# Kernel tuning notes

Measured on AMD Instinct MI355X. Metric: run time of the kernel, lower is better.

The kernel has to match this reference:

```python
import jax, jax.numpy as jnp
import numpy as np

B, N, D, H, F = 16, 512, 768, 12, 3072
HD = D // H
EPS = 1e-5
NEG_INF = -1e30  # stand-in for -inf; softmax of all -inf rows handled via nan_to_num semantics


def layer_norm(x, g, b):
    mu = jnp.mean(x, axis=-1, keepdims=True)
    var = jnp.mean(jnp.square(x - mu), axis=-1, keepdims=True)
    return (x - mu) * jax.lax.rsqrt(var + EPS) * g + b


def setup_inputs() -> dict:
    key = jax.random.key(0)
    ks = jax.random.split(key, 16)
    s = 0.02
    return {
        "x": jax.random.normal(ks[0], (B, N, D), jnp.float32),
        "spatial_encoding": jax.random.normal(ks[1], (B, N, N), jnp.float32),
        "edge_encoding": jax.random.normal(ks[2], (B, N, N), jnp.float32),
        "Wq": jax.random.normal(ks[3], (D, D), jnp.float32) * s,
        "Wk": jax.random.normal(ks[4], (D, D), jnp.float32) * s,
        "Wv": jax.random.normal(ks[5], (D, D), jnp.float32) * s,
        "bv": jnp.zeros((D,), jnp.float32),
        "Wo": jax.random.normal(ks[6], (D, D), jnp.float32) * s,
        "bo": jnp.zeros((D,), jnp.float32),
        "g1": jnp.ones((D,), jnp.float32),
        "be1": jnp.zeros((D,), jnp.float32),
        "g2": jnp.ones((D,), jnp.float32),
        "be2": jnp.zeros((D,), jnp.float32),
        "W1": jax.random.normal(ks[7], (D, F), jnp.float32) * s,
        "bf1": jnp.zeros((F,), jnp.float32),
        "W2": jax.random.normal(ks[8], (F, D), jnp.float32) * s,
        "bf2": jnp.zeros((D,), jnp.float32),
    }


def reference(x, spatial_encoding, edge_encoding, Wq, Wk, Wv, bv, Wo, bo,
              g1, be1, g2, be2, W1, bf1, W2, bf2):
    scale = D ** (-0.5)
    h = layer_norm(x, g1, be1)                              # n1(x)
    bias = (spatial_encoding + edge_encoding)[:, None]      # [B,1,N,N]

    q = (h @ Wq).reshape(B, N, H, HD).transpose(0, 2, 1, 3)  # [B,H,N,hd]
    k = (h @ Wk).reshape(B, N, H, HD).transpose(0, 2, 1, 3)
    v = (h @ Wv + bv).reshape(B, N, H, HD).transpose(0, 2, 1, 3)

    a = jnp.einsum('bhqd,bhkd->bhqk', q, k) * scale + bias   # [B,H,N,N]
    # pad rows (all-zero score rows) get -inf -> softmax NaN -> nan_to_num -> 0
    row_nonzero = jnp.any(a != 0, axis=-1, keepdims=True)
    a = jnp.where(row_nonzero, a, NEG_INF)
    p = jax.nn.softmax(a, axis=-1)
    p = jnp.where(row_nonzero, p, 0.0)  # mirrors nan_to_num on all -inf rows

    o = jnp.einsum('bhqk,bhkd->bhqd', p, v)                  # [B,H,N,hd]
    o = o.transpose(0, 2, 1, 3).reshape(B, N, D)
    att_output = o @ Wo + bo + x                              # residual

    pad_mask = jnp.any(att_output == 0, axis=-1)              # [B,N]
    ffn_in = layer_norm(x, g2, be2)                           # note: n2(x), as in source
    hmid = jax.nn.gelu(ffn_in @ W1 + bf1, approximate=True)
    ffn_out = hmid @ W2 + bf2 + att_output
    return jnp.where(pad_mask[..., None], 0.0, ffn_out)
```

## Files before the change

### kernel.cpp

```cpp
#include <hip/hip_runtime.h>
#include <math.h>

typedef unsigned short u16;
typedef __bf16 bf16x8 __attribute__((ext_vector_type(8)));
typedef float f32x4 __attribute__((ext_vector_type(4)));

__device__ __forceinline__ u16 f2bf(float f){
  union{float f; unsigned u;} v; v.f = f;
  return (u16)((v.u + 0x7fffu + ((v.u >> 16) & 1u)) >> 16);
}
__device__ __forceinline__ float bf2f(u16 b){
  union{unsigned u; float f;} v; v.u = (unsigned)b << 16; return v.f;
}

#define LOG2E 1.4426950408889634f

__global__ void prep_weights(const float* __restrict__ Wq, const float* __restrict__ Wk,
                             const float* __restrict__ Wv, const float* __restrict__ Wo,
                             const float* __restrict__ W1, const float* __restrict__ W2,
                             const float* __restrict__ g1, const float* __restrict__ g2,
                             u16* __restrict__ WqkvT, u16* __restrict__ WoT,
                             u16* __restrict__ W1T, u16* __restrict__ W2T, float qscale){
  __shared__ float t[32][33];
  int bid = blockIdx.x;
  const float* src; u16* dst; const float* rs; float sc; int R, C, bx, by;
  if (bid < 576)      {            src=Wq; dst=WqkvT;          rs=g1;      sc=qscale; R=768;  C=768;  bx=bid%24; by=bid/24; }
  else if (bid <1152) { bid-=576;  src=Wk; dst=WqkvT+768*768;  rs=g1;      sc=1.f;    R=768;  C=768;  bx=bid%24; by=bid/24; }
  else if (bid <1728) { bid-=1152; src=Wv; dst=WqkvT+1536*768; rs=g1;      sc=1.f;    R=768;  C=768;  bx=bid%24; by=bid/24; }
  else if (bid <2304) { bid-=1728; src=Wo; dst=WoT;            rs=nullptr; sc=1.f;    R=768;  C=768;  bx=bid%24; by=bid/24; }
  else if (bid <4608) { bid-=2304; src=W1; dst=W1T;            rs=g2;      sc=1.f;    R=768;  C=3072; bx=bid%96; by=bid/96; }
  else                { bid-=4608; src=W2; dst=W2T;            rs=nullptr; sc=1.f;    R=3072; C=768;  bx=bid%24; by=bid/24; }
  int c0 = bx * 32, r0 = by * 32;
  int tx = threadIdx.x, ty = threadIdx.y;
  #pragma unroll
  for (int i = 0; i < 4; i++)
    t[ty + i*8][tx] = src[(size_t)(r0 + ty + i*8) * C + c0 + tx];
  __syncthreads();
  float fac = (rs ? rs[r0 + tx] : 1.f) * sc;
  #pragma unroll
  for (int i = 0; i < 4; i++)
    dst[(size_t)(c0 + ty + i*8) * R + r0 + tx] = f2bf(t[tx][ty + i*8] * fac);
}

__global__ __launch_bounds__(256) void fold_bias(
    const float* __restrict__ Wq, const float* __restrict__ Wk,
    const float* __restrict__ Wv, const float* __restrict__ W1,
    const float* __restrict__ be1, const float* __restrict__ be2,
    const float* __restrict__ bv, const float* __restrict__ bf1,
    float* __restrict__ qkvb, float* __restrict__ bf1f){
  __shared__ float red[4][64];
  int tx = threadIdx.x & 63, ty = threadIdx.x >> 6;
  int j = blockIdx.x * 64 + tx;
  const float* W; int col, stride; const float* bvec;
  if (j < 768)       { W = Wq; col = j;        stride = 768;  bvec = be1; }
  else if (j < 1536) { W = Wk; col = j - 768;  stride = 768;  bvec = be1; }
  else if (j < 2304) { W = Wv; col = j - 1536; stride = 768;  bvec = be1; }
  else               { W = W1; col = j - 2304; stride = 3072; bvec = be2; }
  float s = 0.f;
  for (int k = ty * 192; k < (ty + 1) * 192; k++)
    s += bvec[k] * W[(size_t)k * stride + col];
  red[ty][tx] = s;
  __syncthreads();
  if (ty == 0){
    s = red[0][tx] + red[1][tx] + red[2][tx] + red[3][tx];
    if (j < 1536)      qkvb[j] = s;
    else if (j < 2304) qkvb[j] = s + bv[col];
    else               bf1f[col] = s + bf1[col];
  }
}

__global__ void bias_prep(u16* __restrict__ dst, const float* __restrict__ sp,
                          const float* __restrict__ ed){
  int t = blockIdx.x * blockDim.x + threadIdx.x;
  int row = t >> 7, c0 = (t & 127) * 4;
  size_t base = (size_t)row * 512;
  float4 s = *(const float4*)&sp[base + c0];
  float4 e = *(const float4*)&ed[base + c0];
  int kt = c0 >> 7, cw = c0 & 127, fk = cw >> 4, l0 = cw & 15;
  u16* o = dst + base + kt*128 + fk;
  o[(l0+0)*8] = f2bf((s.x+e.x)*LOG2E);
  o[(l0+1)*8] = f2bf((s.y+e.y)*LOG2E);
  o[(l0+2)*8] = f2bf((s.z+e.z)*LOG2E);
  o[(l0+3)*8] = f2bf((s.w+e.w)*LOG2E);
}

__global__ __launch_bounds__(256) void ln_kernel(
    const float* __restrict__ x, u16* __restrict__ hn){
  const int lane = threadIdx.x & 63, wave = threadIdx.x >> 6;
  const int row = blockIdx.x * 4 + wave;
  const float4* xr = (const float4*)(x + (size_t)row * 768);
  float4 v[3];
  float sum = 0.f, sq = 0.f;
  #pragma unroll
  for (int c = 0; c < 3; c++){
    v[c] = xr[lane + 64*c];
    sum += v[c].x + v[c].y + v[c].z + v[c].w;
    sq  += v[c].x*v[c].x + v[c].y*v[c].y + v[c].z*v[c].z + v[c].w*v[c].w;
  }
  #pragma unroll
  for (int d = 1; d < 64; d <<= 1){ sum += __shfl_xor(sum, d); sq += __shfl_xor(sq, d); }
  float mu  = sum * (1.f/768.f);
  float var = sq * (1.f/768.f) - mu*mu;
  float rs  = rsqrtf(var + 1e-5f);
  #pragma unroll
  for (int c = 0; c < 3; c++){
    int f4 = lane + 64*c;
    ushort4 o{f2bf((v[c].x-mu)*rs), f2bf((v[c].y-mu)*rs),
              f2bf((v[c].z-mu)*rs), f2bf((v[c].w-mu)*rs)};
    ((ushort4*)(hn + (size_t)row*768))[f4] = o;
  }
}

template<int EPI>
__global__ __launch_bounds__(256, 2) void gemm_bt(
    const u16* __restrict__ A, const u16* __restrict__ Bt, void* __restrict__ Cout,
    const float* __restrict__ bias, const void* __restrict__ resid,
    u16* __restrict__ vt, int M, int Nn, int K){
  __shared__ __align__(16) u16 As[128*64];
  __shared__ __align__(16) u16 Bs[128*64];
  const int tid = threadIdx.x, lane = tid & 63, wave = tid >> 6;
  const int wm = wave >> 1, wn = wave & 1;
  const int l15 = lane & 15, lg = lane >> 4;
  const int bid = blockIdx.y * gridDim.x + blockIdx.x;
  const int cpx = (gridDim.x * gridDim.y) >> 3;
  const int swz = (bid & 7) * cpx + (bid >> 3);
  const int m0 = (swz / gridDim.x) * 128, n0 = (swz % gridDim.x) * 128;
  f32x4 acc[4][4] = {};
  for (int k0 = 0; k0 < K; k0 += 64){
    #pragma unroll
    for (int i = 0; i < 4; i++){
      int chunk = i*256 + tid;
      int row = chunk >> 3, seg = (chunk & 7) ^ (row & 7);
      __builtin_amdgcn_global_load_lds(
        (const __attribute__((address_space(1))) void*)&A[(size_t)(m0+row)*K + k0 + seg*8],
        (__attribute__((address_space(3))) void*)&As[(size_t)(i*256 + wave*64)*8], 16, 0, 0);
      __builtin_amdgcn_global_load_lds(
        (const __attribute__((address_space(1))) void*)&Bt[(size_t)(n0+row)*K + k0 + seg*8],
        (__attribute__((address_space(3))) void*)&Bs[(size_t)(i*256 + wave*64)*8], 16, 0, 0);
    }
    __syncthreads();
    bf16x8 af[4][2], bfr[4][2];
    #pragma unroll
    for (int i = 0; i < 4; i++){
      int ra = wm*64 + i*16 + l15, rb = wn*64 + i*16 + l15;
      #pragma unroll
      for (int kk = 0; kk < 2; kk++){
        af[i][kk]  = *(const bf16x8*)&As[ra*64 + (((kk*4 + lg) ^ (l15 & 7)) << 3)];
        bfr[i][kk] = *(const bf16x8*)&Bs[rb*64 + (((kk*4 + lg) ^ (l15 & 7)) << 3)];
      }
    }
    #pragma unroll
    for (int kk = 0; kk < 2; kk++)
      #pragma unroll
      for (int i = 0; i < 4; i++)
        #pragma unroll
        for (int j = 0; j < 4; j++)
          acc[i][j] = __builtin_amdgcn_mfma_f32_16x16x32_bf16(af[i][kk], bfr[j][kk], acc[i][j], 0, 0, 0);
    __syncthreads();
  }
  #pragma unroll
  for (int i = 0; i < 4; i++){
    int row_base = m0 + wm*64 + i*16 + lg*4;
    #pragma unroll
    for (int j = 0; j < 4; j++){
      int col = n0 + wn*64 + j*16 + l15;
      float bcol = bias ? bias[col] : 0.f;
      if (EPI == 5 && col >= 1536){
        int hv = (col - 1536) >> 6, hd = (col - 1536) & 63;
        int b = row_base >> 9, n = row_base & 511;
        int within = n & 127;
        int newn = (n & ~127) + ((((within >> 3) ^ (hd & 7)) << 3)) + (within & 7);
        ushort4 ov{f2bf(acc[i][j][0] + bcol), f2bf(acc[i][j][1] + bcol),
                   f2bf(acc[i][j][2] + bcol), f2bf(acc[i][j][3] + bcol)};
        *(ushort4*)&vt[(((size_t)(b*12 + hv)*64 + hd) << 9) + newn] = ov;
        continue;
      }
      #pragma unroll
      for (int r = 0; r < 4; r++){
        size_t idx = (size_t)(row_base + r) * Nn + col;
        float v = acc[i][j][r] + bcol;
        if (EPI == 3){
          v += ((const float*)resid)[idx];
          ((u16*)Cout)[idx] = f2bf(v);
        } else if (EPI == 4){
          v += bf2f(((const u16*)resid)[idx]);
          ((float*)Cout)[idx] = v;
        } else if (EPI == 2){
          float u = v + 0.044715f * v * v * v;
          float e = exp2f(-2.3022182f * u);
          ((u16*)Cout)[idx] = f2bf(v * __builtin_amdgcn_rcpf(1.f + e));
        } else {
          ((u16*)Cout)[idx] = f2bf(v);
        }
      }
    }
  }
}

__device__ __forceinline__ void attn_body(
    int bid, u16* sm, const u16* __restrict__ qkv, const u16* __restrict__ VTg,
    const u16* __restrict__ biasPb, u16* __restrict__ Og){
  u16* Ks = sm;
  u16* Vs = sm + 8192;
  u16* Pl = sm + 16384;
  const int tid = threadIdx.x, lane = tid & 63, wave = tid >> 6;
  const int l15 = lane & 15, lg = lane >> 4;
  const int swz = (bid & 7) * 96 + (bid >> 3);
  const int bh = swz >> 2, b = bh / 12, h = bh % 12;
  const int q0 = (swz & 3) * 128 + wave * 32;
  const u16* Qb = qkv + (size_t)b * 512 * 2304 + h * 64;
  const u16* Kb = Qb + 768;
  const u16* Vbh = VTg + (size_t)bh * 64 * 512;
  u16* Pw = &Pl[wave * 32 * 136];

  bf16x8 qf[2][2];
  #pragma unroll
  for (int fm = 0; fm < 2; fm++)
    #pragma unroll
    for (int kk = 0; kk < 2; kk++)
      qf[fm][kk] = *(const bf16x8*)&Qb[(size_t)(q0 + fm*16 + l15)*2304 + kk*32 + lg*8];

  f32x4 O[2][4] = {};
  float lrow[2][4] = {};

  for (int kt = 0; kt < 4; kt++){
    const int k0 = kt * 128;
    bf16x8 bb[2][4];
    #pragma unroll
    for (int fm = 0; fm < 2; fm++)
      #pragma unroll
      for (int r = 0; r < 4; r++){
        int qrow = q0 + fm*16 + lg*4 + r;
        bb[fm][r] = *(const bf16x8*)&biasPb[((size_t)(b*512 + qrow)*4 + kt)*128 + l15*8];
      }
    #pragma unroll
    for (int i = 0; i < 4; i++){
      int chunk = i*256 + tid;
      int r = chunk >> 3, cc = chunk & 7;
      __builtin_amdgcn_global_load_lds(
        (const __attribute__((address_space(1))) void*)&Kb[(size_t)(k0 + r)*2304 + ((cc ^ (r & 7)) << 3)],
        (__attribute__((address_space(3))) void*)&Ks[(size_t)(i*256 + wave*64)*8],
        16, 0, 0);
    }
    #pragma unroll
    for (int i = 0; i < 4; i++){
      int chunk = i*256 + tid;
      int r = chunk >> 4, cc = chunk & 15;
      __builtin_amdgcn_global_load_lds(
        (const __attribute__((address_space(1))) void*)&Vbh[(size_t)r*512 + k0 + (cc << 3)],
        (__attribute__((address_space(3))) void*)&Vs[(size_t)(i*256 + wave*64)*8],
        16, 0, 0);
    }
    __syncthreads();

    f32x4 S[2][8] = {};
    #pragma unroll
    for (int fk = 0; fk < 8; fk++)
      #pragma unroll
      for (int kk = 0; kk < 2; kk++){
        int row = fk*16 + l15;
        bf16x8 kf = *(const bf16x8*)&Ks[row*64 + (((kk*4 + lg) ^ (l15 & 7)) << 3)];
        S[0][fk] = __builtin_amdgcn_mfma_f32_16x16x32_bf16(qf[0][kk], kf, S[0][fk], 0,0,0);
        S[1][fk] = __builtin_amdgcn_mfma_f32_16x16x32_bf16(qf[1][kk], kf, S[1][fk], 0,0,0);
      }
    #pragma unroll
    for (int fm = 0; fm < 2; fm++)
      #pragma unroll
      for (int r = 0; r < 4; r++){
        float rs = 0.f;
        #pragma unroll
        for (int fk = 0; fk < 8; fk++){
          float p = exp2f(S[fm][fk][r] + (float)bb[fm][r][fk]);
          S[fm][fk][r] = p;
          rs += p;
        }
        rs += __shfl_xor(rs, 1); rs += __shfl_xor(rs, 2);
        rs += __shfl_xor(rs, 4); rs += __shfl_xor(rs, 8);
        lrow[fm][r] += rs;
      }
    #pragma unroll
    for (int fm = 0; fm < 2; fm++)
      #pragma unroll
      for (int fk = 0; fk < 8; fk++)
        #pragma unroll
        for (int r = 0; r < 4; r++)
          Pw[(fm*16 + lg*4 + r)*136 + fk*16 + l15] = f2bf(S[fm][fk][r]);
    bf16x8 pf[2][4];
    #pragma unroll
    for (int fm = 0; fm < 2; fm++)
      #pragma unroll
      for (int kk = 0; kk < 4; kk++)
        pf[fm][kk] = *(const bf16x8*)&Pw[(fm*16 + l15)*136 + kk*32 + lg*8];
    #pragma unroll
    for (int fn = 0; fn < 4; fn++)
      #pragma unroll
      for (int kk = 0; kk < 4; kk++){
        int row = fn*16 + l15;
        bf16x8 vf = *(const bf16x8*)&Vs[row*128 + (((kk*4 + lg) ^ (l15 & 7)) << 3)];
        O[0][fn] = __builtin_amdgcn_mfma_f32_16x16x32_bf16(pf[0][kk], vf, O[0][fn], 0,0,0);
        O[1][fn] = __builtin_amdgcn_mfma_f32_16x16x32_bf16(pf[1][kk], vf, O[1][fn], 0,0,0);
      }
    __syncthreads();
  }
  #pragma unroll
  for (int fm = 0; fm < 2; fm++)
    #pragma unroll
    for (int r = 0; r < 4; r++){
      float inv = __builtin_amdgcn_rcpf(lrow[fm][r]);
      int qrow = q0 + fm*16 + lg*4 + r;
      #pragma unroll
      for (int fn = 0; fn < 4; fn++)
        Og[((size_t)b*512 + qrow)*768 + h*64 + fn*16 + l15] = f2bf(O[fm][fn][r] * inv);
    }
}

__device__ __forceinline__ void ffn1_body(
    int fid, u16* sm, const u16* __restrict__ A, const u16* __restrict__ Bt,
    u16* __restrict__ Cout, const float* __restrict__ bias){
  u16* As = sm;
  u16* Bs = sm + 8192;
  const int Nn = 3072, K = 768;
  const int tid = threadIdx.x, lane = tid & 63, wave = tid >> 6;
  const int wm = wave >> 1, wn = wave & 1;
  const int l15 = lane & 15, lg = lane >> 4;
  const int swz = (fid & 7) * 192 + (fid >> 3);
  const int m0 = (swz / 24) * 128, n0 = (swz % 24) * 128;
  f32x4 acc[4][4] = {};
  for (int k0 = 0; k0 < K; k0 += 64){
    #pragma unroll
    for (int i = 0; i < 4; i++){
      int chunk = i*256 + tid;
      int row = chunk >> 3, seg = (chunk & 7) ^ (row & 7);
      __builtin_amdgcn_global_load_lds(
        (const __attribute__((address_space(1))) void*)&A[(size_t)(m0+row)*K + k0 + seg*8],
        (__attribute__((address_space(3))) void*)&As[(size_t)(i*256 + wave*64)*8], 16, 0, 0);
      __builtin_amdgcn_global_load_lds(
        (const __attribute__((address_space(1))) void*)&Bt[(size_t)(n0+row)*K + k0 + seg*8],
        (__attribute__((address_space(3))) void*)&Bs[(size_t)(i*256 + wave*64)*8], 16, 0, 0);
    }
    __syncthreads();
    bf16x8 af[4][2], bfr[4][2];
    #pragma unroll
    for (int i = 0; i < 4; i++){
      int ra = wm*64 + i*16 + l15, rb = wn*64 + i*16 + l15;
      #pragma unroll
      for (int kk = 0; kk < 2; kk++){
        af[i][kk]  = *(const bf16x8*)&As[ra*64 + (((kk*4 + lg) ^ (l15 & 7)) << 3)];
        bfr[i][kk] = *(const bf16x8*)&Bs[rb*64 + (((kk*4 + lg) ^ (l15 & 7)) << 3)];
      }
    }
    #pragma unroll
    for (int kk = 0; kk < 2; kk++)
      #pragma unroll
      for (int i = 0; i < 4; i++)
        #pragma unroll
        for (int j = 0; j < 4; j++)
          acc[i][j] = __builtin_amdgcn_mfma_f32_16x16x32_bf16(af[i][kk], bfr[j][kk], acc[i][j], 0, 0, 0);
    __syncthreads();
  }
  #pragma unroll
  for (int i = 0; i < 4; i++){
    int row_base = m0 + wm*64 + i*16 + lg*4;
    #pragma unroll
    for (int j = 0; j < 4; j++){
      int col = n0 + wn*64 + j*16 + l15;
      float bcol = bias[col];
      #pragma unroll
      for (int r = 0; r < 4; r++){
        size_t idx = (size_t)(row_base + r) * Nn + col;
        float v = acc[i][j][r] + bcol;
        float u = v + 0.044715f * v * v * v;
        float e = exp2f(-2.3022182f * u);
        Cout[idx] = f2bf(v * __builtin_amdgcn_rcpf(1.f + e));
      }
    }
  }
}

__global__ __launch_bounds__(256, 2) void attn_ffn1(
    const u16* __restrict__ qkv, const u16* __restrict__ VTg,
    const u16* __restrict__ biasPb, u16* __restrict__ Og,
    const u16* __restrict__ hn, const u16* __restrict__ W1T,
    u16* __restrict__ Gg, const float* __restrict__ bf1f){
  __shared__ __align__(16) u16 sm[33792];
  const int bid = blockIdx.x;
  const int t = bid / 3, r = bid - t * 3;
  if (r == 0) attn_body(t, sm, qkv, VTg, biasPb, Og);
  else        ffn1_body(2*t + (r-1), sm, hn, W1T, Gg, bf1f);
}

extern "C" void kernel_launch(void* const* d_in, const int* in_sizes, int n_in,
                              void* d_out, int out_size, void* d_ws, size_t ws_size,
                              hipStream_t stream){
  const float* x   = (const float*)d_in[0];
  const float* sp  = (const float*)d_in[1];
  const float* ed  = (const float*)d_in[2];
  const float* Wq  = (const float*)d_in[3];
  const float* Wk  = (const float*)d_in[4];
  const float* Wv  = (const float*)d_in[5];
  const float* bv  = (const float*)d_in[6];
  const float* Wo  = (const float*)d_in[7];
  const float* bo  = (const float*)d_in[8];
  const float* g1  = (const float*)d_in[9];
  const float* be1 = (const float*)d_in[10];
  const float* g2  = (const float*)d_in[11];
  const float* be2 = (const float*)d_in[12];
  const float* W1  = (const float*)d_in[13];
  const float* bf1 = (const float*)d_in[14];
  const float* W2  = (const float*)d_in[15];
  const float* bf2 = (const float*)d_in[16];

  char* w = (char*)d_ws;
  size_t off = 0;
  auto alloc = [&](size_t bytes)->void*{ void* p = w + off; off += (bytes + 255) & ~(size_t)255; return p; };
  u16*   Gg    = (u16*)  alloc(8192ull*3072*2);
  u16*   qkv   = (u16*)  alloc(8192ull*2304*2);
  u16*   attb  = qkv;
  u16*   VTg   = (u16*)  alloc(8192ull*768*2);
  u16*   hn    = (u16*)  alloc(8192ull*768*2);
  u16*   Og    = (u16*)  alloc(8192ull*768*2);
  u16*   biasPb= (u16*)  alloc(16ull*512*512*2);
  u16*   WqkvT = (u16*)  alloc(2304ull*768*2);
  u16*   WoT   = (u16*)  alloc(768ull*768*2);
  u16*   W1T   = (u16*)  alloc(3072ull*768*2);
  u16*   W2T   = (u16*)  alloc(768ull*3072*2);
  float* qkvb  = (float*)alloc(2304ull*4);
  float* bf1f  = (float*)alloc(3072ull*4);

  const float qscale = 0.03608439182435161f * LOG2E;

  prep_weights<<<6912, dim3(32,8), 0, stream>>>(Wq, Wk, Wv, Wo, W1, W2, g1, g2,
                                                WqkvT, WoT, W1T, W2T, qscale);
  fold_bias<<<84, 256, 0, stream>>>(Wq, Wk, Wv, W1, be1, be2, bv, bf1, qkvb, bf1f);
  bias_prep<<<4096, 256, 0, stream>>>(biasPb, sp, ed);

  ln_kernel<<<2048, 256, 0, stream>>>(x, hn);

  gemm_bt<5><<<dim3(18,64),256,0,stream>>>(hn, WqkvT, qkv, qkvb, nullptr, VTg, 8192, 2304, 768);

  attn_ffn1<<<2304, 256, 0, stream>>>(qkv, VTg, biasPb, Og, hn, W1T, Gg, bf1f);

  gemm_bt<3><<<dim3(6,64),256,0,stream>>>(Og, WoT, attb, bo, x, nullptr, 8192, 768, 768);

  gemm_bt<4><<<dim3(6,64),256,0,stream>>>(Gg, W2T, (float*)d_out, bf2, attb, nullptr, 8192, 768, 3072);
}
```

Before: 255.3 us.

## Merge prep kernels and fuse Wo and W2 GEMMs into one concatenated-K GEMM

Combines bias prep, weight transpose, bias folding and LayerNorm into a single launch with block-range dispatch. The output projection and the second FFN GEMM become one GEMM that loops over a concatenated K range (Gg·W2T then Og·WoT). The epilogue adds the folded bias bo+bf2 and the residual x directly. This removes the bf16 attb intermediate round-trip and two kernel launches. The trade-off is a longer serial K loop per tile and a dispatch-heavy prep kernel.

```diff
diff --git a/kernel.cpp b/kernel.cpp
--- a/kernel.cpp
+++ b/kernel.cpp
@@ -9,113 +9,117 @@
   union{float f; unsigned u;} v; v.f = f;
   return (u16)((v.u + 0x7fffu + ((v.u >> 16) & 1u)) >> 16);
 }
-__device__ __forceinline__ float bf2f(u16 b){
-  union{unsigned u; float f;} v; v.u = (unsigned)b << 16; return v.f;
-}
 
 #define LOG2E 1.4426950408889634f
 
-__global__ void prep_weights(const float* __restrict__ Wq, const float* __restrict__ Wk,
-                             const float* __restrict__ Wv, const float* __restrict__ Wo,
-                             const float* __restrict__ W1, const float* __restrict__ W2,
-                             const float* __restrict__ g1, const float* __restrict__ g2,
-                             u16* __restrict__ WqkvT, u16* __restrict__ WoT,
-                             u16* __restrict__ W1T, u16* __restrict__ W2T, float qscale){
-  __shared__ float t[32][33];
-  int bid = blockIdx.x;
-  const float* src; u16* dst; const float* rs; float sc; int R, C, bx, by;
-  if (bid < 576)      {            src=Wq; dst=WqkvT;          rs=g1;      sc=qscale; R=768;  C=768;  bx=bid%24; by=bid/24; }
-  else if (bid <1152) { bid-=576;  src=Wk; dst=WqkvT+768*768;  rs=g1;      sc=1.f;    R=768;  C=768;  bx=bid%24; by=bid/24; }
-  else if (bid <1728) { bid-=1152; src=Wv; dst=WqkvT+1536*768; rs=g1;      sc=1.f;    R=768;  C=768;  bx=bid%24; by=bid/24; }
-  else if (bid <2304) { bid-=1728; src=Wo; dst=WoT;            rs=nullptr; sc=1.f;    R=768;  C=768;  bx=bid%24; by=bid/24; }
-  else if (bid <4608) { bid-=2304; src=W1; dst=W1T;            rs=g2;      sc=1.f;    R=768;  C=3072; bx=bid%96; by=bid/96; }
-  else                { bid-=4608; src=W2; dst=W2T;            rs=nullptr; sc=1.f;    R=3072; C=768;  bx=bid%24; by=bid/24; }
-  int c0 = bx * 32, r0 = by * 32;
-  int tx = threadIdx.x, ty = threadIdx.y;
-  #pragma unroll
-  for (int i = 0; i < 4; i++)
-    t[ty + i*8][tx] = src[(size_t)(r0 + ty + i*8) * C + c0 + tx];
-  __syncthreads();
-  float fac = (rs ? rs[r0 + tx] : 1.f) * sc;
-  #pragma unroll
-  for (int i = 0; i < 4; i++)
-    dst[(size_t)(c0 + ty + i*8) * R + r0 + tx] = f2bf(t[tx][ty + i*8] * fac);
-}
-
-__global__ __launch_bounds__(256) void fold_bias(
+__global__ __launch_bounds__(256) void prep_all(
+    const float* __restrict__ sp, const float* __restrict__ ed,
     const float* __restrict__ Wq, const float* __restrict__ Wk,
-    const float* __restrict__ Wv, const float* __restrict__ W1,
+    const float* __restrict__ Wv, const float* __restrict__ Wo,
+    const float* __restrict__ W1, const float* __restrict__ W2,
+    const float* __restrict__ g1, const float* __restrict__ g2,
     const float* __restrict__ be1, const float* __restrict__ be2,
     const float* __restrict__ bv, const float* __restrict__ bf1,
-    float* __restrict__ qkvb, float* __restrict__ bf1f){
+    const float* __restrict__ bo, const float* __restrict__ bf2,
+    const float* __restrict__ x,
+    u16* __restrict__ biasPb, u16* __restrict__ WqkvT, u16* __restrict__ WoT,
+    u16* __restrict__ W1T, u16* __restrict__ W2T,
+    float* __restrict__ qkvb, float* __restrict__ bf1f, float* __restrict__ bo2,
+    u16* __restrict__ hn, float qscale){
+  __shared__ float t[32][33];
   __shared__ float red[4][64];
-  int tx = threadIdx.x & 63, ty = threadIdx.x >> 6;
-  int j = blockIdx.x * 64 + tx;
-  const float* W; int col, stride; const float* bvec;
-  if (j < 768)       { W = Wq; col = j;        stride = 768;  bvec = be1; }
-  else if (j < 1536) { W = Wk; col = j - 768;  stride = 768;  bvec = be1; }
-  else if (j < 2304) { W = Wv; col = j - 1536; stride = 768;  bvec = be1; }
-  else               { W = W1; col = j - 2304; stride = 3072; bvec = be2; }
-  float s = 0.f;
-  for (int k = ty * 192; k < (ty + 1) * 192; k++)
-    s += bvec[k] * W[(size_t)k * stride + col];
-  red[ty][tx] = s;
-  __syncthreads();
-  if (ty == 0){
-    s = red[0][tx] + red[1][tx] + red[2][tx] + red[3][tx];
-    if (j < 1536)      qkvb[j] = s;
-    else if (j < 2304) qkvb[j] = s + bv[col];
-    else               bf1f[col] = s + bf1[col];
-  }
-}
-
-__global__ void bias_prep(u16* __restrict__ dst, const float* __restrict__ sp,
-                          const float* __restrict__ ed){
-  int t = blockIdx.x * blockDim.x + threadIdx.x;
-  int row = t >> 7, c0 = (t & 127) * 4;
-  size_t base = (size_t)row * 512;
-  float4 s = *(const float4*)&sp[base + c0];
-  float4 e = *(const float4*)&ed[base + c0];
-  int kt = c0 >> 7, cw = c0 & 127, fk = cw >> 4, l0 = cw & 15;
-  u16* o = dst + base + kt*128 + fk;
-  o[(l0+0)*8] = f2bf((s.x+e.x)*LOG2E);
-  o[(l0+1)*8] = f2bf((s.y+e.y)*LOG2E);
-  o[(l0+2)*8] = f2bf((s.z+e.z)*LOG2E);
-  o[(l0+3)*8] = f2bf((s.w+e.w)*LOG2E);
-}
-
-__global__ __launch_bounds__(256) void ln_kernel(
-    const float* __restrict__ x, u16* __restrict__ hn){
-  const int lane = threadIdx.x & 63, wave = threadIdx.x >> 6;
-  const int row = blockIdx.x * 4 + wave;
-  const float4* xr = (const float4*)(x + (size_t)row * 768);
-  float4 v[3];
-  float sum = 0.f, sq = 0.f;
-  #pragma unroll
-  for (int c = 0; c < 3; c++){
-    v[c] = xr[lane + 64*c];
-    sum += v[c].x + v[c].y + v[c].z + v[c].w;
-    sq  += v[c].x*v[c].x + v[c].y*v[c].y + v[c].z*v[c].z + v[c].w*v[c].w;
-  }
-  #pragma unroll
-  for (int d = 1; d < 64; d <<= 1){ sum += __shfl_xor(sum, d); sq += __shfl_xor(sq, d); }
-  float mu  = sum * (1.f/768.f);
-  float var = sq * (1.f/768.f) - mu*mu;
-  float rs  = rsqrtf(var + 1e-5f);
-  #pragma unroll
-  for (int c = 0; c < 3; c++){
-    int f4 = lane + 64*c;
-    ushort4 o{f2bf((v[c].x-mu)*rs), f2bf((v[c].y-mu)*rs),
-              f2bf((v[c].z-mu)*rs), f2bf((v[c].w-mu)*rs)};
-    ((ushort4*)(hn + (size_t)row*768))[f4] = o;
-  }
-}
-
-template<int EPI>
-__global__ __launch_bounds__(256, 2) void gemm_bt(
-    const u16* __restrict__ A, const u16* __restrict__ Bt, void* __restrict__ Cout,
-    const float* __restrict__ bias, const void* __restrict__ resid,
-    u16* __restrict__ vt, int M, int Nn, int K){
+  const int gbid = blockIdx.x, tid = threadIdx.x;
+
+  if (gbid < 4096){
+    int tt = gbid * 256 + tid;
+    int row = tt >> 7, c0 = (tt & 127) * 4;
+    size_t base = (size_t)row * 512;
+    float4 s = *(const float4*)&sp[base + c0];
+    float4 e = *(const float4*)&ed[base + c0];
+    int kt = c0 >> 7, cw = c0 & 127, fk = cw >> 4, l0 = cw & 15;
+    u16* o = biasPb + base + kt*128 + fk;
+    o[(l0+0)*8] = f2bf((s.x+e.x)*LOG2E);
+    o[(l0+1)*8] = f2bf((s.y+e.y)*LOG2E);
+    o[(l0+2)*8] = f2bf((s.z+e.z)*LOG2E);
+    o[(l0+3)*8] = f2bf((s.w+e.w)*LOG2E);
+  } else if (gbid < 11008){
+    int bid = gbid - 4096;
+    const float* src; u16* dst; const float* rs; float sc; int R, C, bx, by;
+    if (bid < 576)      {            src=Wq; dst=WqkvT;          rs=g1;      sc=qscale; R=768;  C=768;  bx=bid%24; by=bid/24; }
+    else if (bid <1152) { bid-=576;  src=Wk; dst=WqkvT+768*768;  rs=g1;      sc=1.f;    R=768;  C=768;  bx=bid%24; by=bid/24; }
+    else if (bid <1728) { bid-=1152; src=Wv; dst=WqkvT+1536*768; rs=g1;      sc=1.f;    R=768;  C=768;  bx=bid%24; by=bid/24; }
+    else if (bid <2304) { bid-=1728; src=Wo; dst=WoT;            rs=nullptr; sc=1.f;    R=768;  C=768;  bx=bid%24; by=bid/24; }
+    else if (bid <4608) { bid-=2304; src=W1; dst=W1T;            rs=g2;      sc=1.f;    R=768;  C=3072; bx=bid%96; by=bid/96; }
+    else                { bid-=4608; src=W2; dst=W2T;            rs=nullptr; sc=1.f;    R=3072; C=768;  bx=bid%24; by=bid/24; }
+    int c0 = bx * 32, r0 = by * 32;
+    int tx = tid & 31, ty = tid >> 5;
+    #pragma unroll
+    for (int i = 0; i < 4; i++)
+      t[ty + i*8][tx] = src[(size_t)(r0 + ty + i*8) * C + c0 + tx];
+    __syncthreads();
+    float fac = (rs ? rs[r0 + tx] : 1.f) * sc;
+    #pragma unroll
+    for (int i = 0; i < 4; i++)
+      dst[(size_t)(c0 + ty + i*8) * R + r0 + tx] = f2bf(t[tx][ty + i*8] * fac);
+  } else if (gbid < 11104){
+    int fbid = gbid - 11008;
+    int tx = tid & 63, ty = tid >> 6;
+    int j = fbid * 64 + tx;
+    if (j < 5376){
+      const float* W; int col, stride; const float* bvec;
+      if (j < 768)       { W = Wq; col = j;        stride = 768;  bvec = be1; }
+      else if (j < 1536) { W = Wk; col = j - 768;  stride = 768;  bvec = be1; }
+      else if (j < 2304) { W = Wv; col = j - 1536; stride = 768;  bvec = be1; }
+      else               { W = W1; col = j - 2304; stride = 3072; bvec = be2; }
+      float s = 0.f;
+      for (int k = ty * 192; k < (ty + 1) * 192; k++)
+        s += bvec[k] * W[(size_t)k * stride + col];
+      red[ty][tx] = s;
+    }
+    __syncthreads();
+    if (ty == 0){
+      if (j < 5376){
+        float s = red[0][tx] + red[1][tx] + red[2][tx] + red[3][tx];
+        if (j < 1536)      qkvb[j] = s;
+        else if (j < 2304) qkvb[j] = s + bv[j - 1536];
+        else               bf1f[j - 2304] = s + bf1[j - 2304];
+      } else {
+        int col = j - 5376;
+        bo2[col] = bo[col] + bf2[col];
+      }
+    }
+  } else {
+    int lbid = gbid - 11104;
+    const int lane = tid & 63, wave = tid >> 6;
+    const int row = lbid * 4 + wave;
+    const float4* xr = (const float4*)(x + (size_t)row * 768);
+    float4 v[3];
+    float sum = 0.f, sq = 0.f;
+    #pragma unroll
+    for (int c = 0; c < 3; c++){
+      v[c] = xr[lane + 64*c];
+      sum += v[c].x + v[c].y + v[c].z + v[c].w;
+      sq  += v[c].x*v[c].x + v[c].y*v[c].y + v[c].z*v[c].z + v[c].w*v[c].w;
+    }
+    #pragma unroll
+    for (int d = 1; d < 64; d <<= 1){ sum += __shfl_xor(sum, d); sq += __shfl_xor(sq, d); }
+    float mu  = sum * (1.f/768.f);
+    float var = sq * (1.f/768.f) - mu*mu;
+    float rs  = rsqrtf(var + 1e-5f);
+    #pragma unroll
+    for (int c = 0; c < 3; c++){
+      int f4 = lane + 64*c;
+      ushort4 o{f2bf((v[c].x-mu)*rs), f2bf((v[c].y-mu)*rs),
+                f2bf((v[c].z-mu)*rs), f2bf((v[c].w-mu)*rs)};
+      ((ushort4*)(hn + (size_t)row*768))[f4] = o;
+    }
+  }
+}
+
+__global__ __launch_bounds__(256, 2) void gemm_qkv(
+    const u16* __restrict__ A, const u16* __restrict__ Bt, u16* __restrict__ Cout,
+    const float* __restrict__ bias, u16* __restrict__ vt){
+  const int Nn = 2304, K = 768;
   __shared__ __align__(16) u16 As[128*64];
   __shared__ __align__(16) u16 Bs[128*64];
   const int tid = threadIdx.x, lane = tid & 63, wave = tid >> 6;
@@ -164,8 +168,8 @@
     #pragma unroll
     for (int j = 0; j < 4; j++){
       int col = n0 + wn*64 + j*16 + l15;
-      float bcol = bias ? bias[col] : 0.f;
-      if (EPI == 5 && col >= 1536){
+      float bcol = bias[col];
+      if (col >= 1536){
         int hv = (col - 1536) >> 6, hd = (col - 1536) & 63;
         int b = row_base >> 9, n = row_base & 511;
         int within = n & 127;
@@ -173,25 +177,10 @@
         ushort4 ov{f2bf(acc[i][j][0] + bcol), f2bf(acc[i][j][1] + bcol),
                    f2bf(acc[i][j][2] + bcol), f2bf(acc[i][j][3] + bcol)};
         *(ushort4*)&vt[(((size_t)(b*12 + hv)*64 + hd) << 9) + newn] = ov;
-        continue;
-      }
-      #pragma unroll
-      for (int r = 0; r < 4; r++){
-        size_t idx = (size_t)(row_base + r) * Nn + col;
-        float v = acc[i][j][r] + bcol;
-        if (EPI == 3){
-          v += ((const float*)resid)[idx];
-          ((u16*)Cout)[idx] = f2bf(v);
-        } else if (EPI == 4){
-          v += bf2f(((const u16*)resid)[idx]);
-          ((float*)Cout)[idx] = v;
-        } else if (EPI == 2){
-          float u = v + 0.044715f * v * v * v;
-          float e = exp2f(-2.3022182f * u);
-          ((u16*)Cout)[idx] = f2bf(v * __builtin_amdgcn_rcpf(1.f + e));
-        } else {
-          ((u16*)Cout)[idx] = f2bf(v);
-        }
+      } else {
+        #pragma unroll
+        for (int r = 0; r < 4; r++)
+          Cout[(size_t)(row_base + r) * Nn + col] = f2bf(acc[i][j][r] + bcol);
       }
     }
   }
@@ -387,6 +376,73 @@
   const int t = bid / 3, r = bid - t * 3;
   if (r == 0) attn_body(t, sm, qkv, VTg, biasPb, Og);
   else        ffn1_body(2*t + (r-1), sm, hn, W1T, Gg, bf1f);
+}
+
+__global__ __launch_bounds__(256, 2) void gemm_fin(
+    const u16* __restrict__ Gg, const u16* __restrict__ Og,
+    const u16* __restrict__ W2T, const u16* __restrict__ WoT,
+    float* __restrict__ Cout, const float* __restrict__ bo2,
+    const float* __restrict__ x){
+  const int Nn = 768;
+  __shared__ __align__(16) u16 As[128*64];
+  __shared__ __align__(16) u16 Bs[128*64];
+  const int tid = threadIdx.x, lane = tid & 63, wave = tid >> 6;
+  const int wm = wave >> 1, wn = wave & 1;
+  const int l15 = lane & 15, lg = lane >> 4;
+  const int bid = blockIdx.y * gridDim.x + blockIdx.x;
+  const int cpx = (gridDim.x * gridDim.y) >> 3;
+  const int swz = (bid & 7) * cpx + (bid >> 3);
+  const int m0 = (swz / gridDim.x) * 128, n0 = (swz % gridDim.x) * 128;
+  f32x4 acc[4][4] = {};
+  for (int k0 = 0; k0 < 3840; k0 += 64){
+    const u16* Ab; const u16* Bb; int str; int kk0;
+    if (k0 < 3072){ Ab = Gg; Bb = W2T; str = 3072; kk0 = k0; }
+    else          { Ab = Og; Bb = WoT; str = 768;  kk0 = k0 - 3072; }
+    #pragma unroll
+    for (int i = 0; i < 4; i++){
+      int chunk = i*256 + tid;
+      int row = chunk >> 3, seg = (chunk & 7) ^ (row & 7);
+      __builtin_amdgcn_global_load_lds(
+        (const __attribute__((address_space(1))) void*)&Ab[(size_t)(m0+row)*str + kk0 + seg*8],
+        (__attribute__((address_space(3))) void*)&As[(size_t)(i*256 + wave*64)*8], 16, 0, 0);
+      __builtin_amdgcn_global_load_lds(
+        (const __attribute__((address_space(1))) void*)&Bb[(size_t)(n0+row)*str + kk0 + seg*8],
+        (__attribute__((address_space(3))) void*)&Bs[(size_t)(i*256 + wave*64)*8], 16, 0, 0);
+    }
+    __syncthreads();
+    bf16x8 af[4][2], bfr[4][2];
+    #pragma unroll
+    for (int i = 0; i < 4; i++){
+      int ra = wm*64 + i*16 + l15, rb = wn*64 + i*16 + l15;
+      #pragma unroll
+      for (int kk = 0; kk < 2; kk++){
+        af[i][kk]  = *(const bf16x8*)&As[ra*64 + (((kk*4 + lg) ^ (l15 & 7)) << 3)];
+        bfr[i][kk] = *(const bf16x8*)&Bs[rb*64 + (((kk*4 + lg) ^ (l15 & 7)) << 3)];
+      }
+    }
+    #pragma unroll
+    for (int kk = 0; kk < 2; kk++)
+      #pragma unroll
+      for (int i = 0; i < 4; i++)
+        #pragma unroll
+        for (int j = 0; j < 4; j++)
+          acc[i][j] = __builtin_amdgcn_mfma_f32_16x16x32_bf16(af[i][kk], bfr[j][kk], acc[i][j], 0, 0, 0);
+    __syncthreads();
+  }
+  #pragma unroll
+  for (int i = 0; i < 4; i++){
+    int row_base = m0 + wm*64 + i*16 + lg*4;
+    #pragma unroll
+    for (int j = 0; j < 4; j++){
+      int col = n0 + wn*64 + j*16 + l15;
+      float bcol = bo2[col];
+      #pragma unroll
+      for (int r = 0; r < 4; r++){
+        size_t idx = (size_t)(row_base + r) * Nn + col;
+        Cout[idx] = acc[i][j][r] + bcol + x[idx];
+      }
+    }
+  }
 }
 
 extern "C" void kernel_launch(void* const* d_in, const int* in_sizes, int n_in,
@@ -415,7 +471,6 @@
   auto alloc = [&](size_t bytes)->void*{ void* p = w + off; off += (bytes + 255) & ~(size_t)255; return p; };
   u16*   Gg    = (u16*)  alloc(8192ull*3072*2);
   u16*   qkv   = (u16*)  alloc(8192ull*2304*2);
-  u16*   attb  = qkv;
   u16*   VTg   = (u16*)  alloc(8192ull*768*2);
   u16*   hn    = (u16*)  alloc(8192ull*768*2);
   u16*   Og    = (u16*)  alloc(8192ull*768*2);
@@ -426,21 +481,18 @@
   u16*   W2T   = (u16*)  alloc(768ull*3072*2);
   float* qkvb  = (float*)alloc(2304ull*4);
   float* bf1f  = (float*)alloc(3072ull*4);
+  float* bo2   = (float*)alloc(768ull*4);
 
   const float qscale = 0.03608439182435161f * LOG2E;
 
-  prep_weights<<<6912, dim3(32,8), 0, stream>>>(Wq, Wk, Wv, Wo, W1, W2, g1, g2,
-                                                WqkvT, WoT, W1T, W2T, qscale);
-  fold_bias<<<84, 256, 0, stream>>>(Wq, Wk, Wv, W1, be1, be2, bv, bf1, qkvb, bf1f);
-  bias_prep<<<4096, 256, 0, stream>>>(biasPb, sp, ed);
-
-  ln_kernel<<<2048, 256, 0, stream>>>(x, hn);
-
-  gemm_bt<5><<<dim3(18,64),256,0,stream>>>(hn, WqkvT, qkv, qkvb, nullptr, VTg, 8192, 2304, 768);
+  prep_all<<<13152, 256, 0, stream>>>(sp, ed, Wq, Wk, Wv, Wo, W1, W2, g1, g2,
+                                      be1, be2, bv, bf1, bo, bf2, x,
+                                      biasPb, WqkvT, WoT, W1T, W2T,
+                                      qkvb, bf1f, bo2, hn, qscale);
+
+  gemm_qkv<<<dim3(18,64),256,0,stream>>>(hn, WqkvT, qkv, qkvb, VTg);
 
   attn_ffn1<<<2304, 256, 0, stream>>>(qkv, VTg, biasPb, Og, hn, W1T, Gg, bf1f);
 
-  gemm_bt<3><<<dim3(6,64),256,0,stream>>>(Og, WoT, attb, bo, x, nullptr, 8192, 768, 768);
-
-  gemm_bt<4><<<dim3(6,64),256,0,stream>>>(Gg, W2T, (float*)d_out, bf2, attb, nullptr, 8192, 768, 3072);
-}
+  gemm_fin<<<dim3(6,64),256,0,stream>>>(Gg, Og, W2T, WoT, (float*)d_out, bo2, x);
+}
```

Result: faster. 234.9 us (-8.0%).
